# Kernel tuning notes

Measured on AMD Instinct MI355X. Metric: run time of the kernel, lower is better.

The kernel has to match this reference:

```python
import jax, jax.numpy as jnp
import numpy as np

D_MODEL = 1024
N_HEADS = 16
D_HEAD = D_MODEL // N_HEADS
LORA_RANK = 8
LORA_ALPHA = 16
LORA_SCALING = LORA_ALPHA / LORA_RANK
NEG_INF = -1.0e9


def setup_inputs() -> dict:
    key = jax.random.key(0)
    ks = jax.random.split(key, 8)
    B, S = 2, 2048
    s_in = 1.0 / np.sqrt(D_MODEL)
    return {
        "x": jax.random.normal(ks[0], (B, S, D_MODEL), dtype=jnp.float32),
        "attention_mask": jnp.ones((B, S), dtype=jnp.int32),
        "W_qkv_kernel": jax.random.normal(ks[1], (D_MODEL, 3 * D_MODEL), jnp.float32) * s_in,
        "W_qkv_bias": jnp.zeros((3 * D_MODEL,), jnp.float32),
        "lora_A_qkv": jax.random.normal(ks[2], (D_MODEL, LORA_RANK), jnp.float32) * 0.01,
        "lora_B_qkv": jax.random.normal(ks[3], (LORA_RANK, 3 * D_MODEL), jnp.float32) * 0.01,
        "c_proj_kernel": jax.random.normal(ks[4], (D_MODEL, D_MODEL), jnp.float32) * s_in,
        "c_proj_bias": jnp.zeros((D_MODEL,), jnp.float32),
        "lora_A_proj": jax.random.normal(ks[5], (D_MODEL, LORA_RANK), jnp.float32) * 0.01,
        "lora_B_proj": jax.random.normal(ks[6], (LORA_RANK, D_MODEL), jnp.float32) * 0.01,
    }


def reference(x, attention_mask, W_qkv_kernel, W_qkv_bias, lora_A_qkv, lora_B_qkv,
              c_proj_kernel, c_proj_bias, lora_A_proj, lora_B_proj):
    B, S, _ = x.shape
    # QKV projection + LoRA adapter
    qkv = x @ W_qkv_kernel + W_qkv_bias
    qkv = qkv + ((x @ lora_A_qkv) @ lora_B_qkv) * LORA_SCALING
    q, k, v = jnp.split(qkv, 3, axis=-1)
    # [B, H, S, Dh]
    q = q.reshape(B, S, N_HEADS, D_HEAD).transpose(0, 2, 1, 3)
    k = k.reshape(B, S, N_HEADS, D_HEAD).transpose(0, 2, 1, 3)
    v = v.reshape(B, S, N_HEADS, D_HEAD).transpose(0, 2, 1, 3)
    # raw scores [B, H, S, S]
    scores = jnp.einsum("bhqd,bhkd->bhqk", q, k)
    # padding mask applied BEFORE scaling (as in the original)
    pad = (attention_mask[:, None, None, :] == 0)
    scores = jnp.where(pad, NEG_INF, scores)
    # causal mask (lower triangular kept)
    causal = jnp.tril(jnp.ones((S, S), dtype=bool))
    scores = jnp.where(causal[None, None, :, :], scores, NEG_INF)
    # scaling applied AFTER masking (faithful to source: -1e9 also divided)
    scaled = scores / jnp.sqrt(jnp.float32(D_HEAD))
    attn = jax.nn.softmax(scaled, axis=-1)
    ctx = jnp.einsum("bhqk,bhkd->bhqd", attn, v)
    ctx = ctx.transpose(0, 2, 1, 3).reshape(B, S, D_MODEL)
    out = ctx @ c_proj_kernel + c_proj_bias
    out = out + ((ctx @ lora_A_proj) @ lora_B_proj) * LORA_SCALING
    return out
```

## Files before the change

### kernel.cpp

```cpp
#include <hip/hip_runtime.h>
#include <hip/hip_bf16.h>

#define LOG2E 1.4426950408889634f
#define MASKVAL (-1.25e8f * LOG2E)

typedef __bf16 bf16x8 __attribute__((ext_vector_type(8)));
typedef __bf16 bf16x4 __attribute__((ext_vector_type(4)));
typedef short  shortx4 __attribute__((ext_vector_type(4)));
typedef float  floatx4 __attribute__((ext_vector_type(4)));

__device__ __forceinline__ floatx4 mfma16(bf16x8 a, bf16x8 b, floatx4 c) {
  return __builtin_amdgcn_mfma_f32_16x16x32_bf16(a, b, c, 0, 0, 0);
}

__device__ __forceinline__ floatx4 mfma_pv(bf16x4 a, bf16x4 b, floatx4 c) {
#if __has_builtin(__builtin_amdgcn_mfma_f32_16x16x16_bf16)
  return __builtin_amdgcn_mfma_f32_16x16x16_bf16(a, b, c, 0, 0, 0);
#else
  shortx4 as, bs;
  __builtin_memcpy(&as, &a, 8);
  __builtin_memcpy(&bs, &b, 8);
  return __builtin_amdgcn_mfma_f32_16x16x16bf16_1k(as, bs, c, 0, 0, 0);
#endif
}

__device__ __forceinline__ void load_lds16(const __bf16* g, __bf16* l) {
  __builtin_amdgcn_global_load_lds(
      (const __attribute__((address_space(1))) void*)g,
      (__attribute__((address_space(3))) void*)l, 16, 0, 0);
}

__device__ __forceinline__ float max3f(float a, float b, float c) {
  return fmaxf(a, fmaxf(b, c));
}

__global__ __launch_bounds__(256)
void fold_wt2(const float* __restrict__ Wq, const float* __restrict__ Aq,
              const float* __restrict__ Bq, __bf16* __restrict__ WTq,
              const float* __restrict__ Wp, const float* __restrict__ Ap,
              const float* __restrict__ Bp, __bf16* __restrict__ WTp) {
  __shared__ float tile[64][65];
  __shared__ float sLb[8][64];
  const int bx = blockIdx.x;
  const bool isQ = bx < 48;
  const float* W  = isQ ? Wq : Wp;
  const float* La = isQ ? Aq : Ap;
  const float* Lb = isQ ? Bq : Bp;
  __bf16* WT = isQ ? WTq : WTp;
  const int ncols = isQ ? 3072 : 1024;
  const int nt = (isQ ? bx : bx - 48) * 64;
  const int kt = blockIdx.y * 64;
  const int tid = threadIdx.x;
  const int tx = tid & 63, ty = tid >> 6;

  float rLa[8];
  *(float4*)&rLa[0] = *(const float4*)(La + (size_t)(kt + tx) * 8);
  *(float4*)&rLa[4] = *(const float4*)(La + (size_t)(kt + tx) * 8 + 4);

#pragma unroll
  for (int rep = 0; rep < 2; rep++) {
    int idx = tid + rep * 256;
    sLb[idx >> 6][idx & 63] = Lb[(size_t)(idx >> 6) * ncols + nt + (idx & 63)];
  }
#pragma unroll
  for (int rep = 0; rep < 16; rep++) {
    int i = rep * 4 + ty;
    tile[i][tx] = W[(size_t)(kt + i) * ncols + nt + tx];
  }
  __syncthreads();
#pragma unroll
  for (int rep = 0; rep < 16; rep++) {
    int i = rep * 4 + ty;
    int n = nt + i, k = kt + tx;
    float acc = tile[tx][i];
#pragma unroll
    for (int r = 0; r < 8; r++)
      acc += 2.0f * rLa[r] * sLb[r][i];
    WT[(size_t)n * 1024 + k] = (__bf16)acc;
  }
}

__global__ __launch_bounds__(256)
void cast_x(const float* __restrict__ x, __bf16* __restrict__ o) {
  int i = blockIdx.x * 256 + threadIdx.x;
  float4 v = ((const float4*)x)[i];
  bf16x4 r = {(__bf16)v.x, (__bf16)v.y, (__bf16)v.z, (__bf16)v.w};
  ((bf16x4*)o)[i] = r;
}

__global__ __launch_bounds__(256)
void gemm_qkv(const __bf16* __restrict__ WT, const __bf16* __restrict__ X,
              const float* __restrict__ bias, __bf16* __restrict__ qk,
              __bf16* __restrict__ vtb) {
  const int K = 1024;
  __shared__ alignas(16) __bf16 smem[32768];
  const int tid = threadIdx.x;
  const int wave = tid >> 6, lane = tid & 63;
  const int wm = wave >> 1, wn = wave & 1;
  const int quad = lane >> 4, l15 = lane & 15;
  const int p0 = blockIdx.y * 128, s0 = blockIdx.x * 128;
  const int srow8 = lane >> 3, sc8 = lane & 7;
  const int sswz = sc8 ^ srow8;

  auto STAGE = [&](int bb, int kb) {
    __bf16* Ab = smem + bb * 8192;
    __bf16* Bb = smem + 16384 + bb * 8192;
#pragma unroll
    for (int t = 0; t < 4; t++) {
      int rbase = (wave * 4 + t) * 8;
      int row = rbase + srow8;
      load_lds16(WT + (size_t)(p0 + row) * K + kb + sswz * 8, Ab + rbase * 64);
      load_lds16(X + (size_t)(s0 + row) * K + kb + sswz * 8, Bb + rbase * 64);
    }
  };

  floatx4 acc[4][4] = {};
  STAGE(0, 0);

  for (int it = 0; it < 16; it++) {
    const int cur = it & 1;
    if (it < 15) {
      STAGE(cur ^ 1, (it + 1) * 64);
      asm volatile("s_waitcnt vmcnt(8)" ::: "memory");
    } else {
      asm volatile("s_waitcnt vmcnt(0)" ::: "memory");
    }
    __builtin_amdgcn_s_barrier();
    __builtin_amdgcn_sched_barrier(0);
    const __bf16* Ac = smem + cur * 8192;
    const __bf16* Bc = smem + 16384 + cur * 8192;
#pragma unroll
    for (int ks = 0; ks < 2; ks++) {
      bf16x8 af[4], bfv[4];
#pragma unroll
      for (int t = 0; t < 4; t++) {
        int ra = wm * 64 + t * 16 + l15;
        int rb = wn * 64 + t * 16 + l15;
        int ch = (ks * 4 + quad) ^ (l15 & 7);
        af[t]  = *(const bf16x8*)(Ac + ra * 64 + ch * 8);
        bfv[t] = *(const bf16x8*)(Bc + rb * 64 + ch * 8);
      }
#pragma unroll
      for (int mi = 0; mi < 4; mi++)
#pragma unroll
        for (int ni = 0; ni < 4; ni++)
          acc[mi][ni] = mfma16(af[mi], bfv[ni], acc[mi][ni]);
    }
    __builtin_amdgcn_s_barrier();
  }

  __bf16* ep = smem;
  const int b = s0 >> 11, s2b = s0 & 2047;

  if (p0 < 2048) {
    const float qscale = (p0 < 1024) ? 0.125f * LOG2E : 1.0f;
#pragma unroll
    for (int mi = 0; mi < 4; mi++) {
      int ch0 = wm * 64 + mi * 16 + quad * 4;
      float4 b4 = *(const float4*)(bias + p0 + ch0);
#pragma unroll
      for (int ni = 0; ni < 4; ni++) {
        int tl = wn * 64 + ni * 16 + l15;
        bf16x4 o = {(__bf16)((acc[mi][ni][0] + b4.x) * qscale),
                    (__bf16)((acc[mi][ni][1] + b4.y) * qscale),
                    (__bf16)((acc[mi][ni][2] + b4.z) * qscale),
                    (__bf16)((acc[mi][ni][3] + b4.w) * qscale)};
        *(bf16x4*)(ep + tl * 136 + ch0) = o;
      }
    }
    __syncthreads();
    const int part = p0 >> 10;
    const int h0 = (p0 & 1023) >> 6;
    const int hs = wave & 1, tb = (wave >> 1) * 64;
    __bf16* outp = qk + (size_t)part * 4194304 +
                   ((size_t)((b * 16 + h0 + hs) * 2048 + s2b)) * 64;
#pragma unroll
    for (int j = 0; j < 8; j++) {
      int tok = tb + j * 8 + (lane >> 3);
      int dh = (lane & 7) * 8;
      bf16x8 v = *(const bf16x8*)(ep + tok * 136 + hs * 64 + dh);
      *(bf16x8*)(outp + (size_t)tok * 64 + dh) = v;
    }
  } else {
#pragma unroll
    for (int mi = 0; mi < 4; mi++) {
      int ch0 = wm * 64 + mi * 16 + quad * 4;
      float4 b4 = *(const float4*)(bias + p0 + ch0);
#pragma unroll
      for (int ni = 0; ni < 4; ni++) {
        int tl = wn * 64 + ni * 16 + l15;
        int off = tl & 63, t = off >> 4, qd = (off >> 2) & 3, rr = off & 3;
        int ptl = (tl & 64) | ((t >> 1) * 32 + qd * 8 + (t & 1) * 4 + rr);
        ep[(ch0 + 0) * 136 + ptl] = (__bf16)(acc[mi][ni][0] + b4.x);
        ep[(ch0 + 1) * 136 + ptl] = (__bf16)(acc[mi][ni][1] + b4.y);
        ep[(ch0 + 2) * 136 + ptl] = (__bf16)(acc[mi][ni][2] + b4.z);
        ep[(ch0 + 3) * 136 + ptl] = (__bf16)(acc[mi][ni][3] + b4.w);
      }
    }
    __syncthreads();
    const int h0 = (p0 & 1023) >> 6;
#pragma unroll
    for (int j = 0; j < 8; j++) {
      int ch = wave * 32 + j * 4 + (lane >> 4);
      int to = (lane & 15) * 8;
      bf16x8 v = *(const bf16x8*)(ep + ch * 136 + to);
      int h = h0 + (ch >> 6), dh = ch & 63;
      *(bf16x8*)(vtb + ((size_t)((b * 16 + h) * 64 + dh)) * 2048 + s2b + to) =
          v;
    }
  }
}

__global__ __launch_bounds__(256)
void gemm_proj(const __bf16* __restrict__ A, const __bf16* __restrict__ BT,
               const float* __restrict__ bias, float* __restrict__ Cout, int N) {
  const int K = 1024;
  __shared__ alignas(16) __bf16 smem[24576];
  const int tid = threadIdx.x;
  const int wave = tid >> 6, lane = tid & 63;
  const int wm = wave >> 1, wn = wave & 1;
  const int quad = lane >> 4, l15 = lane & 15;
  const int m0 = blockIdx.y * 64, n0 = blockIdx.x * 128;
  const int srow8 = lane >> 3, sc8 = lane & 7;
  const int sswz = sc8 ^ srow8;

  auto STAGE = [&](int bb, int kb) {
    __bf16* Ab = smem + bb * 4096;
    __bf16* Bb = smem + 8192 + bb * 8192;
#pragma unroll
    for (int t = 0; t < 2; t++) {
      int rbase = (wave * 2 + t) * 8;
      load_lds16(A + (size_t)(m0 + rbase + srow8) * K + kb + sswz * 8,
                 Ab + rbase * 64);
    }
#pragma unroll
    for (int t = 0; t < 4; t++) {
      int rbase = (wave * 4 + t) * 8;
      load_lds16(BT + (size_t)(n0 + rbase + srow8) * K + kb + sswz * 8,
                 Bb + rbase * 64);
    }
  };

  floatx4 acc[2][4] = {};
  STAGE(0, 0);

  for (int it = 0; it < 16; it++) {
    const int cur = it & 1;
    if (it < 15) {
      STAGE(cur ^ 1, (it + 1) * 64);
      asm volatile("s_waitcnt vmcnt(6)" ::: "memory");
    } else {
      asm volatile("s_waitcnt vmcnt(0)" ::: "memory");
    }
    __builtin_amdgcn_s_barrier();
    __builtin_amdgcn_sched_barrier(0);
    const __bf16* Ac = smem + cur * 4096;
    const __bf16* Bc = smem + 8192 + cur * 8192;
#pragma unroll
    for (int ks = 0; ks < 2; ks++) {
      bf16x8 af[2], bfv[4];
      int ch = (ks * 4 + quad) ^ (l15 & 7);
#pragma unroll
      for (int t = 0; t < 2; t++)
        af[t] = *(const bf16x8*)(Ac + (wm * 32 + t * 16 + l15) * 64 + ch * 8);
#pragma unroll
      for (int t = 0; t < 4; t++)
        bfv[t] = *(const bf16x8*)(Bc + (wn * 64 + t * 16 + l15) * 64 + ch * 8);
#pragma unroll
      for (int mi = 0; mi < 2; mi++)
#pragma unroll
        for (int ni = 0; ni < 4; ni++)
          acc[mi][ni] = mfma16(af[mi], bfv[ni], acc[mi][ni]);
    }
    __builtin_amdgcn_s_barrier();
  }

#pragma unroll
  for (int mi = 0; mi < 2; mi++)
#pragma unroll
    for (int ni = 0; ni < 4; ni++) {
      int n = n0 + wn * 64 + ni * 16 + l15;
#pragma unroll
      for (int r = 0; r < 4; r++) {
        int m = m0 + wm * 32 + mi * 16 + quad * 4 + r;
        Cout[(size_t)m * N + n] = acc[mi][ni][r] + bias[n];
      }
    }
}

__global__ __launch_bounds__(256)
void flash_attn(const __bf16* __restrict__ q, const __bf16* __restrict__ k,
                const __bf16* __restrict__ vt, const int* __restrict__ amask,
                __bf16* __restrict__ ctx) {
  const int S = 2048;
  __shared__ alignas(16) __bf16 Ks[2][64 * 64];
  __shared__ alignas(16) __bf16 Vs[2][64 * 64];
  const int bid = blockIdx.x;
  const int jb = 31 - (bid >> 5);
  const int bh = bid & 31;
  const int b = bh >> 4, h = bh & 15;
  const int wave = threadIdx.x >> 6, lane = threadIdx.x & 63;
  const int quad = lane >> 4, l15 = lane & 15;
  const int srow8 = lane >> 3, sc8 = lane & 7;
  const int sswz = sc8 ^ srow8;
  const int Q0 = jb * 64;
  const int qrow = Q0 + wave * 16 + l15;

  const __bf16* qp  = q  + (size_t)bh * S * 64;
  const __bf16* kp0 = k  + (size_t)bh * S * 64;
  const __bf16* vp0 = vt + (size_t)bh * 64 * S;

  int anyp = 0;
  const int npre = (jb + 4) >> 2;
  for (int it = 0; it < npre; it++) {
    int4 v = *(const int4*)(amask + b * S + it * 256 + lane * 4);
    anyp |= (v.x == 0) | (v.y == 0) | (v.z == 0) | (v.w == 0);
  }
  const bool padded = (__ballot(anyp) != 0ull);

  bf16x8 qf[2];
#pragma unroll
  for (int ks = 0; ks < 2; ks++)
    qf[ks] = *(const bf16x8*)(qp + (size_t)qrow * 64 + ks * 32 + quad * 8);

  auto STAGE = [&](int bb, int cc) {
#pragma unroll
    for (int t = 0; t < 2; t++) {
      int rbase = (wave * 2 + t) * 8;
      load_lds16(kp0 + (size_t)cc * 4096 + (size_t)(rbase + srow8) * 64 +
                     sswz * 8,
                 &Ks[bb][rbase * 64]);
    }
#pragma unroll
    for (int t = 0; t < 2; t++) {
      int rbase = (wave * 2 + t) * 8;
      load_lds16(vp0 + (size_t)(rbase + srow8) * S + cc * 64 + sswz * 8,
                 &Vs[bb][rbase * 64]);
    }
  };

  STAGE(0, 0);

  float mrun = 0.0f, lrun = 0.0f;
  floatx4 oacc[4] = {};

  for (int c = 0; c <= jb; c++) {
    const int cur = c & 1;
    if (c < jb) {
      STAGE(cur ^ 1, c + 1);
      asm volatile("s_waitcnt vmcnt(4)" ::: "memory");
    } else {
      asm volatile("s_waitcnt vmcnt(0)" ::: "memory");
    }
    __builtin_amdgcn_s_barrier();
    __builtin_amdgcn_sched_barrier(0);

    floatx4 st[4] = {};
    __builtin_amdgcn_s_setprio(1);
#pragma unroll
    for (int ks = 0; ks < 2; ks++) {
      const int ch = (ks * 4 + quad) ^ (l15 & 7);
      bf16x8 kf[4];
#pragma unroll
      for (int nt = 0; nt < 4; nt++)
        kf[nt] = *(const bf16x8*)(&Ks[cur][(nt * 16 + l15) * 64 + ch * 8]);
#pragma unroll
      for (int nt = 0; nt < 4; nt++)
        st[nt] = mfma16(kf[nt], qf[ks], st[nt]);
    }
    __builtin_amdgcn_s_setprio(0);

    if (padded) {
      int am_c = amask[b * S + c * 64 + lane];
      unsigned long long pm = __ballot(am_c == 0);
#pragma unroll
      for (int nt = 0; nt < 4; nt++) {
        int kl = nt * 16 + quad * 4;
#pragma unroll
        for (int r = 0; r < 4; r++) {
          bool pad = (pm >> (kl + r)) & 1ull;
          bool masked = pad || ((c == jb) && (kl + r > wave * 16 + l15));
          st[nt][r] = masked ? MASKVAL : st[nt][r];
        }
      }
    } else if (c == jb) {
#pragma unroll
      for (int nt = 0; nt < 4; nt++) {
        int kl = nt * 16 + quad * 4;
#pragma unroll
        for (int r = 0; r < 4; r++) {
          bool masked = kl + r > wave * 16 + l15;
          st[nt][r] = masked ? MASKVAL : st[nt][r];
        }
      }
    }

    float t0 = max3f(st[0][0], st[0][1], st[0][2]);
    float t1 = max3f(st[0][3], st[1][0], st[1][1]);
    float t2 = max3f(st[1][2], st[1][3], st[2][0]);
    float t3 = max3f(st[2][1], st[2][2], st[2][3]);
    float t4 = max3f(st[3][0], st[3][1], st[3][2]);
    float inm = fmaxf(max3f(t0, t1, t2), max3f(t3, t4, st[3][3]));
#pragma unroll
    for (int nt = 0; nt < 4; nt++)
#pragma unroll
      for (int r = 0; r < 4; r++)
        st[nt][r] = exp2f(st[nt][r] - mrun);
    float ssum = (((st[0][0] + st[0][1]) + (st[0][2] + st[0][3])) +
                  ((st[1][0] + st[1][1]) + (st[1][2] + st[1][3]))) +
                 (((st[2][0] + st[2][1]) + (st[2][2] + st[2][3])) +
                  ((st[3][0] + st[3][1]) + (st[3][2] + st[3][3])));
    if (!__all(inm - mrun <= 8.0f)) {
      float rm = fmaxf(inm, __shfl_xor(inm, 16, 64));
      rm = fmaxf(rm, __shfl_xor(rm, 32, 64));
      float mnew = fmaxf(mrun, rm);
      float al = exp2f(mrun - mnew);
      mrun = mnew;
      lrun *= al;
      ssum *= al;
#pragma unroll
      for (int nt = 0; nt < 4; nt++)
#pragma unroll
        for (int r = 0; r < 4; r++) st[nt][r] *= al;
#pragma unroll
      for (int nd = 0; nd < 4; nd++)
#pragma unroll
        for (int r = 0; r < 4; r++) oacc[nd][r] *= al;
    }
    lrun += ssum;

    bf16x4 pB[4];
#pragma unroll
    for (int nt = 0; nt < 4; nt++) {
      bf16x4 pk = {(__bf16)st[nt][0], (__bf16)st[nt][1],
                   (__bf16)st[nt][2], (__bf16)st[nt][3]};
      pB[nt] = pk;
    }

    __builtin_amdgcn_s_setprio(1);
#pragma unroll
    for (int tp = 0; tp < 2; tp++) {
      const int chv = (tp * 4 + quad) ^ (l15 & 7);
#pragma unroll
      for (int nd = 0; nd < 4; nd++) {
        bf16x8 v8 =
            *(const bf16x8*)(&Vs[cur][(nd * 16 + l15) * 64 + chv * 8]);
        bf16x4 vA0 = {v8[0], v8[1], v8[2], v8[3]};
        bf16x4 vA1 = {v8[4], v8[5], v8[6], v8[7]};
        oacc[nd] = mfma_pv(vA0, pB[2 * tp], oacc[nd]);
        oacc[nd] = mfma_pv(vA1, pB[2 * tp + 1], oacc[nd]);
      }
    }
    __builtin_amdgcn_s_setprio(0);

    __builtin_amdgcn_s_barrier();
  }

  lrun += __shfl_xor(lrun, 16, 64);
  lrun += __shfl_xor(lrun, 32, 64);

  const float linv = 1.0f / lrun;
#pragma unroll
  for (int nd = 0; nd < 4; nd++) {
    bf16x4 o = {(__bf16)(oacc[nd][0] * linv), (__bf16)(oacc[nd][1] * linv),
                (__bf16)(oacc[nd][2] * linv), (__bf16)(oacc[nd][3] * linv)};
    *(bf16x4*)(ctx + ((size_t)(b * 2048 + qrow)) * 1024 + h * 64 + nd * 16 +
               quad * 4) = o;
  }
}

extern "C" void kernel_launch(void* const* d_in, const int* in_sizes, int n_in,
                              void* d_out, int out_size, void* d_ws, size_t ws_size,
                              hipStream_t stream) {
  const float* x  = (const float*)d_in[0];
  const int*   am = (const int*)d_in[1];
  const float* Wq = (const float*)d_in[2];
  const float* bq = (const float*)d_in[3];
  const float* Aq = (const float*)d_in[4];
  const float* Bq = (const float*)d_in[5];
  const float* Wp = (const float*)d_in[6];
  const float* bp = (const float*)d_in[7];
  const float* Ap = (const float*)d_in[8];
  const float* Bp = (const float*)d_in[9];

  __bf16* wqkvT = (__bf16*)d_ws;
  __bf16* wpT   = wqkvT + (size_t)3072 * 1024;
  __bf16* xbf   = wpT   + (size_t)1024 * 1024;
  __bf16* qbuf  = xbf   + (size_t)4096 * 1024;
  __bf16* vtbuf = qbuf  + (size_t)2 * 4194304;
  __bf16* ctxb  = vtbuf + (size_t)4194304;

  fold_wt2<<<dim3(64, 16), 256, 0, stream>>>(Wq, Aq, Bq, wqkvT,
                                             Wp, Ap, Bp, wpT);
  cast_x<<<4096, 256, 0, stream>>>(x, xbf);

  gemm_qkv<<<dim3(32, 24), 256, 0, stream>>>(wqkvT, xbf, bq, qbuf, vtbuf);
  flash_attn<<<1024, 256, 0, stream>>>(qbuf, qbuf + 4194304, vtbuf, am, ctxb);
  gemm_proj<<<dim3(8, 64), 256, 0, stream>>>(ctxb, wpT, bp, (float*)d_out, 1024);
}
```

Baseline: 187.2 us.

## Process two adjacent query blocks per attention workgroup to share K/V tiles

Each flash-attention workgroup now handles two consecutive 64-row query blocks (2u and 2u+1), so every staged K/V tile in LDS feeds two sets of QK and PV MFMAs. The odd block's extra diagonal chunk is handled in a separate epilogue step. The grid is halved and blocks are ordered to interleave long and short causal workloads. This cuts global-to-LDS traffic and barrier count per unit of work, at the cost of doubled accumulator registers (possible occupancy loss) and fewer workgroups.

Result: slower. 196.9 us (+5.2%).

```diff
diff --git a/kernel.cpp b/kernel.cpp
--- a/kernel.cpp
+++ b/kernel.cpp
@@ -296,32 +296,36 @@
   __shared__ alignas(16) __bf16 Ks[2][64 * 64];
   __shared__ alignas(16) __bf16 Vs[2][64 * 64];
   const int bid = blockIdx.x;
-  const int jb = 31 - (bid >> 5);
+  const int g = bid >> 5;
+  const int u = (g < 8) ? (15 - g) : (g - 8);
+  const int jA = 2 * u + 1, jB = 2 * u;
   const int bh = bid & 31;
   const int b = bh >> 4, h = bh & 15;
   const int wave = threadIdx.x >> 6, lane = threadIdx.x & 63;
   const int quad = lane >> 4, l15 = lane & 15;
   const int srow8 = lane >> 3, sc8 = lane & 7;
   const int sswz = sc8 ^ srow8;
-  const int Q0 = jb * 64;
-  const int qrow = Q0 + wave * 16 + l15;
+  const int qrowA = jA * 64 + wave * 16 + l15;
+  const int qrowB = jB * 64 + wave * 16 + l15;
 
   const __bf16* qp  = q  + (size_t)bh * S * 64;
   const __bf16* kp0 = k  + (size_t)bh * S * 64;
   const __bf16* vp0 = vt + (size_t)bh * 64 * S;
 
   int anyp = 0;
-  const int npre = (jb + 4) >> 2;
+  const int npre = (jA + 4) >> 2;
   for (int it = 0; it < npre; it++) {
     int4 v = *(const int4*)(amask + b * S + it * 256 + lane * 4);
     anyp |= (v.x == 0) | (v.y == 0) | (v.z == 0) | (v.w == 0);
   }
   const bool padded = (__ballot(anyp) != 0ull);
 
-  bf16x8 qf[2];
-#pragma unroll
-  for (int ks = 0; ks < 2; ks++)
-    qf[ks] = *(const bf16x8*)(qp + (size_t)qrow * 64 + ks * 32 + quad * 8);
+  bf16x8 qfA[2], qfB[2];
+#pragma unroll
+  for (int ks = 0; ks < 2; ks++) {
+    qfA[ks] = *(const bf16x8*)(qp + (size_t)qrowA * 64 + ks * 32 + quad * 8);
+    qfB[ks] = *(const bf16x8*)(qp + (size_t)qrowB * 64 + ks * 32 + quad * 8);
+  }
 
   auto STAGE = [&](int bb, int cc) {
 #pragma unroll
@@ -341,35 +345,12 @@
 
   STAGE(0, 0);
 
-  float mrun = 0.0f, lrun = 0.0f;
-  floatx4 oacc[4] = {};
-
-  for (int c = 0; c <= jb; c++) {
-    const int cur = c & 1;
-    if (c < jb) {
-      STAGE(cur ^ 1, c + 1);
-      asm volatile("s_waitcnt vmcnt(4)" ::: "memory");
-    } else {
-      asm volatile("s_waitcnt vmcnt(0)" ::: "memory");
-    }
-    __builtin_amdgcn_s_barrier();
-    __builtin_amdgcn_sched_barrier(0);
-
-    floatx4 st[4] = {};
-    __builtin_amdgcn_s_setprio(1);
-#pragma unroll
-    for (int ks = 0; ks < 2; ks++) {
-      const int ch = (ks * 4 + quad) ^ (l15 & 7);
-      bf16x8 kf[4];
-#pragma unroll
-      for (int nt = 0; nt < 4; nt++)
-        kf[nt] = *(const bf16x8*)(&Ks[cur][(nt * 16 + l15) * 64 + ch * 8]);
-#pragma unroll
-      for (int nt = 0; nt < 4; nt++)
-        st[nt] = mfma16(kf[nt], qf[ks], st[nt]);
-    }
-    __builtin_amdgcn_s_setprio(0);
-
+  float mrunA = 0.0f, lrunA = 0.0f;
+  float mrunB = 0.0f, lrunB = 0.0f;
+  floatx4 oaccA[4] = {}, oaccB[4] = {};
+
+  auto MASKSM = [&](floatx4 (&st)[4], float& mrun, float& lrun,
+                    floatx4 (&oacc)[4], bf16x4 (&pB)[4], int c, int jX) {
     if (padded) {
       int am_c = amask[b * S + c * 64 + lane];
       unsigned long long pm = __ballot(am_c == 0);
@@ -379,11 +360,11 @@
 #pragma unroll
         for (int r = 0; r < 4; r++) {
           bool pad = (pm >> (kl + r)) & 1ull;
-          bool masked = pad || ((c == jb) && (kl + r > wave * 16 + l15));
+          bool masked = pad || ((c == jX) && (kl + r > wave * 16 + l15));
           st[nt][r] = masked ? MASKVAL : st[nt][r];
         }
       }
-    } else if (c == jb) {
+    } else if (c == jX) {
 #pragma unroll
       for (int nt = 0; nt < 4; nt++) {
         int kl = nt * 16 + quad * 4;
@@ -429,13 +410,41 @@
     }
     lrun += ssum;
 
-    bf16x4 pB[4];
 #pragma unroll
     for (int nt = 0; nt < 4; nt++) {
       bf16x4 pk = {(__bf16)st[nt][0], (__bf16)st[nt][1],
                    (__bf16)st[nt][2], (__bf16)st[nt][3]};
       pB[nt] = pk;
     }
+  };
+
+  for (int c = 0; c <= jB; c++) {
+    const int cur = c & 1;
+    STAGE(cur ^ 1, c + 1);
+    asm volatile("s_waitcnt vmcnt(4)" ::: "memory");
+    __builtin_amdgcn_s_barrier();
+    __builtin_amdgcn_sched_barrier(0);
+
+    floatx4 stA[4] = {}, stB[4] = {};
+    __builtin_amdgcn_s_setprio(1);
+#pragma unroll
+    for (int ks = 0; ks < 2; ks++) {
+      const int ch = (ks * 4 + quad) ^ (l15 & 7);
+      bf16x8 kf[4];
+#pragma unroll
+      for (int nt = 0; nt < 4; nt++)
+        kf[nt] = *(const bf16x8*)(&Ks[cur][(nt * 16 + l15) * 64 + ch * 8]);
+#pragma unroll
+      for (int nt = 0; nt < 4; nt++) {
+        stA[nt] = mfma16(kf[nt], qfA[ks], stA[nt]);
+        stB[nt] = mfma16(kf[nt], qfB[ks], stB[nt]);
+      }
+    }
+    __builtin_amdgcn_s_setprio(0);
+
+    bf16x4 pBA[4], pBB[4];
+    MASKSM(stA, mrunA, lrunA, oaccA, pBA, c, jA);
+    MASKSM(stB, mrunB, lrunB, oaccB, pBB, c, jB);
 
     __builtin_amdgcn_s_setprio(1);
 #pragma unroll
@@ -447,8 +456,10 @@
             *(const bf16x8*)(&Vs[cur][(nd * 16 + l15) * 64 + chv * 8]);
         bf16x4 vA0 = {v8[0], v8[1], v8[2], v8[3]};
         bf16x4 vA1 = {v8[4], v8[5], v8[6], v8[7]};
-        oacc[nd] = mfma_pv(vA0, pB[2 * tp], oacc[nd]);
-        oacc[nd] = mfma_pv(vA1, pB[2 * tp + 1], oacc[nd]);
+        oaccA[nd] = mfma_pv(vA0, pBA[2 * tp], oaccA[nd]);
+        oaccB[nd] = mfma_pv(vA0, pBB[2 * tp], oaccB[nd]);
+        oaccA[nd] = mfma_pv(vA1, pBA[2 * tp + 1], oaccA[nd]);
+        oaccB[nd] = mfma_pv(vA1, pBB[2 * tp + 1], oaccB[nd]);
       }
     }
     __builtin_amdgcn_s_setprio(0);
@@ -456,16 +467,65 @@
     __builtin_amdgcn_s_barrier();
   }
 
-  lrun += __shfl_xor(lrun, 16, 64);
-  lrun += __shfl_xor(lrun, 32, 64);
-
-  const float linv = 1.0f / lrun;
+  {
+    const int c = jA;
+    const int cur = c & 1;
+    asm volatile("s_waitcnt vmcnt(0)" ::: "memory");
+    __builtin_amdgcn_s_barrier();
+    __builtin_amdgcn_sched_barrier(0);
+
+    floatx4 stA[4] = {};
+    __builtin_amdgcn_s_setprio(1);
+#pragma unroll
+    for (int ks = 0; ks < 2; ks++) {
+      const int ch = (ks * 4 + quad) ^ (l15 & 7);
+      bf16x8 kf[4];
+#pragma unroll
+      for (int nt = 0; nt < 4; nt++)
+        kf[nt] = *(const bf16x8*)(&Ks[cur][(nt * 16 + l15) * 64 + ch * 8]);
+#pragma unroll
+      for (int nt = 0; nt < 4; nt++)
+        stA[nt] = mfma16(kf[nt], qfA[ks], stA[nt]);
+    }
+    __builtin_amdgcn_s_setprio(0);
+
+    bf16x4 pBA[4];
+    MASKSM(stA, mrunA, lrunA, oaccA, pBA, c, jA);
+
+    __builtin_amdgcn_s_setprio(1);
+#pragma unroll
+    for (int tp = 0; tp < 2; tp++) {
+      const int chv = (tp * 4 + quad) ^ (l15 & 7);
+#pragma unroll
+      for (int nd = 0; nd < 4; nd++) {
+        bf16x8 v8 =
+            *(const bf16x8*)(&Vs[cur][(nd * 16 + l15) * 64 + chv * 8]);
+        bf16x4 vA0 = {v8[0], v8[1], v8[2], v8[3]};
+        bf16x4 vA1 = {v8[4], v8[5], v8[6], v8[7]};
+        oaccA[nd] = mfma_pv(vA0, pBA[2 * tp], oaccA[nd]);
+        oaccA[nd] = mfma_pv(vA1, pBA[2 * tp + 1], oaccA[nd]);
+      }
+    }
+    __builtin_amdgcn_s_setprio(0);
+  }
+
+  lrunA += __shfl_xor(lrunA, 16, 64);
+  lrunA += __shfl_xor(lrunA, 32, 64);
+  lrunB += __shfl_xor(lrunB, 16, 64);
+  lrunB += __shfl_xor(lrunB, 32, 64);
+
+  const float linvA = 1.0f / lrunA;
+  const float linvB = 1.0f / lrunB;
 #pragma unroll
   for (int nd = 0; nd < 4; nd++) {
-    bf16x4 o = {(__bf16)(oacc[nd][0] * linv), (__bf16)(oacc[nd][1] * linv),
-                (__bf16)(oacc[nd][2] * linv), (__bf16)(oacc[nd][3] * linv)};
-    *(bf16x4*)(ctx + ((size_t)(b * 2048 + qrow)) * 1024 + h * 64 + nd * 16 +
-               quad * 4) = o;
+    bf16x4 oA = {(__bf16)(oaccA[nd][0] * linvA), (__bf16)(oaccA[nd][1] * linvA),
+                 (__bf16)(oaccA[nd][2] * linvA), (__bf16)(oaccA[nd][3] * linvA)};
+    *(bf16x4*)(ctx + ((size_t)(b * 2048 + qrowA)) * 1024 + h * 64 + nd * 16 +
+               quad * 4) = oA;
+    bf16x4 oB = {(__bf16)(oaccB[nd][0] * linvB), (__bf16)(oaccB[nd][1] * linvB),
+                 (__bf16)(oaccB[nd][2] * linvB), (__bf16)(oaccB[nd][3] * linvB)};
+    *(bf16x4*)(ctx + ((size_t)(b * 2048 + qrowB)) * 1024 + h * 64 + nd * 16 +
+               quad * 4) = oB;
   }
 }
 
@@ -495,6 +555,6 @@
   cast_x<<<4096, 256, 0, stream>>>(x, xbf);
 
   gemm_qkv<<<dim3(32, 24), 256, 0, stream>>>(wqkvT, xbf, bq, qbuf, vtbuf);
-  flash_attn<<<1024, 256, 0, stream>>>(qbuf, qbuf + 4194304, vtbuf, am, ctxb);
+  flash_attn<<<512, 256, 0, stream>>>(qbuf, qbuf + 4194304, vtbuf, am, ctxb);
   gemm_proj<<<dim3(8, 64), 256, 0, stream>>>(ctxb, wpT, bp, (float*)d_out, 1024);
 }
```
